# Kernel optimization log

Measured on AMD Instinct MI355X. Metric: run time of the kernel, lower is better.

The kernel has to match this reference:

```python
import jax, jax.numpy as jnp
import numpy as np

N, E, G = 50000, 1600000, 64          # nodes, edges, graphs
NODE_IN, EDGE_IN, HID, L, H = 32, 16, 64, 3, 4
C = HID // H                           # per-head channels (PyG out_channels)


def setup_inputs() -> dict:
    key = jax.random.key(0)
    ks = jax.random.split(key, 12)
    x = jax.random.normal(ks[0], (N, NODE_IN), jnp.float32)
    edge_index = jax.random.randint(ks[1], (2, E), 0, N, jnp.int32)
    edge_attr = jax.random.normal(ks[2], (E, EDGE_IN), jnp.float32)
    batch = jnp.sort(jax.random.randint(ks[3], (N,), 0, G, jnp.int32))
    s = lambda k, shape, fan: jax.random.normal(k, shape, jnp.float32) / np.sqrt(fan)
    Wn = s(ks[4], (NODE_IN, HID), NODE_IN); bn = jnp.zeros((HID,), jnp.float32)
    Wq = s(ks[5], (L, HID, HID), HID);      bq = jnp.zeros((L, HID), jnp.float32)
    Wk = s(ks[6], (L, HID, HID), HID);      bk = jnp.zeros((L, HID), jnp.float32)
    Wv = s(ks[7], (L, HID, HID), HID);      bv = jnp.zeros((L, HID), jnp.float32)
    We = s(ks[8], (L, EDGE_IN, HID), EDGE_IN)          # lin_edge, bias=False in PyG
    Ws = s(ks[9], (L, HID, HID), HID);      bs = jnp.zeros((L, HID), jnp.float32)  # lin_skip
    W1 = s(ks[10], (HID, HID // 2), HID);   b1 = jnp.zeros((HID // 2,), jnp.float32)
    W2 = s(ks[11], (HID // 2, 1), HID // 2); b2 = jnp.zeros((1,), jnp.float32)
    return dict(x=x, edge_index=edge_index, edge_attr=edge_attr, batch=batch,
                Wn=Wn, bn=bn, Wq=Wq, bq=bq, Wk=Wk, bk=bk, Wv=Wv, bv=bv,
                We=We, Ws=Ws, bs=bs, W1=W1, b1=b1, W2=W2, b2=b2)


def _transformer_conv(x, src, dst, edge_attr, Wq, bq, Wk, bk, Wv, bv, We, Ws, bs):
    # PyG TransformerConv (concat=True, beta=False, root_weight=True), eval mode.
    q = (x @ Wq + bq)[dst].reshape(E, H, C)              # query at target nodes
    e = (edge_attr @ We).reshape(E, H, C)                # edge embedding
    k = (x @ Wk + bk)[src].reshape(E, H, C) + e          # key at source + edge
    alpha = (q * k).sum(-1) / jnp.sqrt(jnp.float32(C))   # [E, H]
    amax = jax.ops.segment_max(alpha, dst, num_segments=N)
    ex = jnp.exp(alpha - amax[dst])
    denom = jax.ops.segment_sum(ex, dst, num_segments=N)
    attn = ex / (denom[dst] + 1e-16)                     # segment softmax over in-edges
    v = (x @ Wv + bv)[src].reshape(E, H, C) + e
    agg = jax.ops.segment_sum((v * attn[..., None]).reshape(E, HID), dst, num_segments=N)
    return agg + x @ Ws + bs                             # skip connection (lin_skip)


def reference(x, edge_index, edge_attr, batch, Wn, bn, Wq, bq, Wk, bk, Wv, bv,
              We, Ws, bs, W1, b1, W2, b2):
    src, dst = edge_index[0], edge_index[1]
    h = jax.nn.relu(x @ Wn + bn)
    for l in range(L):  # dropout is identity in eval mode
        h_new = jax.nn.relu(_transformer_conv(h, src, dst, edge_attr,
                                              Wq[l], bq[l], Wk[l], bk[l],
                                              Wv[l], bv[l], We[l], Ws[l], bs[l]))
        h = h + h_new
    # global_mean_pool
    cnt = jax.ops.segment_sum(jnp.ones((N,), h.dtype), batch, num_segments=G)
    pooled = jax.ops.segment_sum(h, batch, num_segments=G) / jnp.maximum(cnt, 1.0)[:, None]
    out = jax.nn.relu(pooled @ W1 + b1) @ W2 + b2
    return out.squeeze(-1)
```

## Files before the change

kernel.cpp:

```cpp
#include <hip/hip_runtime.h>
#include <hip/hip_fp16.h>
#include <stdint.h>

#define Nn 50000
#define Ee 1600000
#define Gg 64
#define TB 2048
#define NTB ((Ee + TB - 1) / TB)
#define NBK ((Nn + 255) / 256)

__global__ void k_hist(const int* __restrict__ ei, int* __restrict__ deg) {
    int e = blockIdx.x * blockDim.x + threadIdx.x;
    if (e < Ee) atomicAdd(&deg[ei[Ee + e]], 1);
}

__global__ void k_scan1(const int* __restrict__ deg, int* __restrict__ row_ptr,
                        int* __restrict__ bsum) {
    __shared__ int buf[256];
    int i = blockIdx.x * 256 + threadIdx.x;
    int v = (i < Nn) ? deg[i] : 0;
    buf[threadIdx.x] = v;
    __syncthreads();
    for (int off = 1; off < 256; off <<= 1) {
        int t = (threadIdx.x >= off) ? buf[threadIdx.x - off] : 0;
        __syncthreads();
        buf[threadIdx.x] += t;
        __syncthreads();
    }
    if (i < Nn) row_ptr[i + 1] = buf[threadIdx.x];
    if (threadIdx.x == 255) bsum[blockIdx.x] = buf[255];
}

__global__ void k_scan2(int* __restrict__ bsum, int nb) {
    __shared__ int buf[256];
    int v = (threadIdx.x < nb) ? bsum[threadIdx.x] : 0;
    buf[threadIdx.x] = v;
    __syncthreads();
    for (int off = 1; off < 256; off <<= 1) {
        int t = (threadIdx.x >= off) ? buf[threadIdx.x - off] : 0;
        __syncthreads();
        buf[threadIdx.x] += t;
        __syncthreads();
    }
    if (threadIdx.x < nb) bsum[threadIdx.x] = buf[threadIdx.x];
}

__global__ void k_scan3(int* __restrict__ row_ptr, const int* __restrict__ bsum) {
    int i = blockIdx.x * 256 + threadIdx.x;
    if (i > Nn) return;
    if (i == 0) { row_ptr[0] = 0; return; }
    int b = (i - 1) >> 8;
    if (b > 0) row_ptr[i] += bsum[b - 1];
}

__global__ void k_scatter(const int* __restrict__ ei, int* __restrict__ cursor,
                          int* __restrict__ src_perm, int* __restrict__ eperm) {
    int e = blockIdx.x * blockDim.x + threadIdx.x;
    if (e >= Ee) return;
    int dst = ei[Ee + e];
    int pos = atomicAdd(&cursor[dst], 1);
    src_perm[pos] = ei[e];
    eperm[pos] = e;
}

__global__ void k_easort(const float* __restrict__ ea, const int* __restrict__ eperm,
                         __half* __restrict__ ea_h) {
    long t = (long)blockIdx.x * blockDim.x + threadIdx.x;
    if (t >= (long)Ee * 4) return;
    long idx = t >> 2;
    int e = eperm[idx];
    float4 v = ((const float4*)ea)[(long)e * 4 + (t & 3)];
    __half2 lo = __floats2half2_rn(v.x, v.y);
    __half2 hi = __floats2half2_rn(v.z, v.w);
    ((__half2*)ea_h)[t * 2]     = lo;
    ((__half2*)ea_h)[t * 2 + 1] = hi;
}


__global__ __launch_bounds__(256) void k_cnt(const int* __restrict__ ei,
                                             int* __restrict__ table) {
    __shared__ int hist[NBK];
    for (int i = threadIdx.x; i < NBK; i += 256) hist[i] = 0;
    __syncthreads();
    int e0 = blockIdx.x * TB;
    for (int i = threadIdx.x; i < TB; i += 256) {
        int e = e0 + i;
        if (e >= Ee) break;
        atomicAdd(&hist[ei[Ee + e] >> 8], 1);
    }
    __syncthreads();
    for (int i = threadIdx.x; i < NBK; i += 256)
        table[i * NTB + blockIdx.x] = hist[i];
}

__global__ __launch_bounds__(256) void k_colscan(int* __restrict__ table,
                                                 int* __restrict__ bktsz) {
    __shared__ int buf[1024];
    int c = blockIdx.x;
    for (int k = 0; k < 4; ++k) {
        int i = threadIdx.x + k * 256;
        buf[i] = (i < NTB) ? table[c * NTB + i] : 0;
    }
    __syncthreads();
    for (int off = 1; off < 1024; off <<= 1) {
        int v[4];
        for (int k = 0; k < 4; ++k) {
            int i = threadIdx.x + k * 256;
            v[k] = (i >= off) ? buf[i - off] : 0;
        }
        __syncthreads();
        for (int k = 0; k < 4; ++k) buf[threadIdx.x + k * 256] += v[k];
        __syncthreads();
    }
    for (int k = 0; k < 4; ++k) {
        int i = threadIdx.x + k * 256;
        if (i < NTB) table[c * NTB + i] = i ? buf[i - 1] : 0;
    }
    if (threadIdx.x == 0) bktsz[c] = buf[1023];
}

__global__ __launch_bounds__(256) void k_bktscan(const int* __restrict__ bktsz,
                                                 int* __restrict__ bktbase) {
    __shared__ int buf[256];
    int i = threadIdx.x;
    buf[i] = (i < NBK) ? bktsz[i] : 0;
    __syncthreads();
    for (int off = 1; off < 256; off <<= 1) {
        int v = (i >= off) ? buf[i - off] : 0;
        __syncthreads();
        buf[i] += v;
        __syncthreads();
    }
    if (i == 0) bktbase[0] = 0;
    if (i < NBK) bktbase[i + 1] = buf[i];
}

__global__ __launch_bounds__(256) void k_binfill(const int* __restrict__ ei,
                        const int* __restrict__ table, const int* __restrict__ bktbase,
                        unsigned long long* __restrict__ tmp) {
    __shared__ int off_s[NBK];
    __shared__ int cnt_s[NBK];
    for (int i = threadIdx.x; i < NBK; i += 256) {
        off_s[i] = table[i * NTB + blockIdx.x];
        cnt_s[i] = 0;
    }
    __syncthreads();
    int e0 = blockIdx.x * TB;
    for (int i = threadIdx.x; i < TB; i += 256) {
        int e = e0 + i;
        if (e >= Ee) break;
        int src = ei[e];
        int dst = ei[Ee + e];
        int b = dst >> 8;
        int r = atomicAdd(&cnt_s[b], 1);
        long pos = (long)bktbase[b] + off_s[b] + r;
        tmp[pos] = ((unsigned long long)(unsigned)dst << 37)
                 | ((unsigned long long)(unsigned)src << 21)
                 | (unsigned long long)(unsigned)e;
    }
}

__global__ __launch_bounds__(256) void k_bktB(const unsigned long long* __restrict__ tmp,
                        const int* __restrict__ bktbase, int* __restrict__ row_ptr,
                        unsigned long long* __restrict__ tmp2) {
    __shared__ int cnt[256];
    __shared__ int sc[256];
    __shared__ int lro[256];
    int b = blockIdx.x, tid = threadIdx.x;
    cnt[tid] = 0;
    __syncthreads();
    int s = bktbase[b], t_end = bktbase[b + 1];
    for (int i = s + tid; i < t_end; i += 256)
        atomicAdd(&cnt[(int)(tmp[i] >> 37) & 255], 1);
    __syncthreads();
    sc[tid] = cnt[tid];
    __syncthreads();
    for (int off = 1; off < 256; off <<= 1) {
        int v = (tid >= off) ? sc[tid - off] : 0;
        __syncthreads();
        sc[tid] += v;
        __syncthreads();
    }
    lro[tid] = tid ? sc[tid - 1] : 0;
    cnt[tid] = 0;
    int n = b * 256 + tid;
    if (n < Nn) row_ptr[n] = s + lro[tid];
    if (b == NBK - 1 && tid == 0) row_ptr[Nn] = Ee;
    __syncthreads();
    for (int i = s + tid; i < t_end; i += 256) {
        unsigned long long p = tmp[i];
        int dn = (int)(p >> 37) & 255;
        int r = atomicAdd(&cnt[dn], 1);
        int pos = s + lro[dn] + r;
        tmp2[pos] = (((p >> 21) & 0xFFFFull) << 32) | (p & 0x1FFFFFull);
    }
}

__global__ void k_scatB(const unsigned long long* __restrict__ tmp2,
                        int* __restrict__ src_perm,
                        const float* __restrict__ ea, __half* __restrict__ ea_h) {
    int t = blockIdx.x * blockDim.x + threadIdx.x;
    if (t >= Ee) return;
    unsigned long long p = tmp2[t];
    src_perm[t] = (int)(p >> 32);
    int e = (int)(p & 0xFFFFFFFFull);
    const float4* er = (const float4*)(ea + (size_t)e * 16);
    float4 v0 = er[0], v1 = er[1], v2 = er[2], v3 = er[3];
    __half2 h0 = __floats2half2_rn(v0.x, v0.y), h1 = __floats2half2_rn(v0.z, v0.w);
    __half2 h2 = __floats2half2_rn(v1.x, v1.y), h3 = __floats2half2_rn(v1.z, v1.w);
    __half2 h4 = __floats2half2_rn(v2.x, v2.y), h5 = __floats2half2_rn(v2.z, v2.w);
    __half2 h6 = __floats2half2_rn(v3.x, v3.y), h7 = __floats2half2_rn(v3.z, v3.w);
    uint4 a = make_uint4(*(unsigned*)&h0, *(unsigned*)&h1,
                         *(unsigned*)&h2, *(unsigned*)&h3);
    uint4 bb = make_uint4(*(unsigned*)&h4, *(unsigned*)&h5,
                          *(unsigned*)&h6, *(unsigned*)&h7);
    uint4* o = (uint4*)(ea_h + (size_t)t * 16);
    o[0] = a;
    o[1] = bb;
}

__global__ void k_gbound(const int* __restrict__ batch, int* __restrict__ gstart) {
    int n = blockIdx.x * blockDim.x + threadIdx.x;
    if (n >= Nn) return;
    int b = batch[n];
    if (n == 0) { for (int g = 0; g <= b; ++g) gstart[g] = 0; }
    else { int bp = batch[n - 1]; for (int g = bp + 1; g <= b; ++g) gstart[g] = n; }
    if (n == Nn - 1) { for (int g = b + 1; g <= Gg; ++g) gstart[g] = Nn; }
}

__global__ __launch_bounds__(256) void k_encode(const float* __restrict__ x,
                         const float* __restrict__ Wn,
                         const float* __restrict__ bn, float* __restrict__ h) {
    __shared__ float sx[64 * 32];
    int base = blockIdx.x * 64;
    for (int i = threadIdx.x; i < 512; i += 256) {
        int off = i * 4, row = off >> 5;
        float4 v = (base + row < Nn) ? ((const float4*)(x))[(base * 32 + off) >> 2]
                                     : make_float4(0.f, 0.f, 0.f, 0.f);
        ((float4*)sx)[i] = v;
    }
    __syncthreads();
    int lane = threadIdx.x & 63, wv = threadIdx.x >> 6;
    float acc[16];
    float b = bn[lane];
#pragma unroll
    for (int nn = 0; nn < 16; ++nn) acc[nn] = b;
#pragma unroll 1
    for (int k0 = 0; k0 < 32; k0 += 4) {
        float w0 = Wn[(k0 + 0) * 64 + lane];
        float w1 = Wn[(k0 + 1) * 64 + lane];
        float w2 = Wn[(k0 + 2) * 64 + lane];
        float w3 = Wn[(k0 + 3) * 64 + lane];
#pragma unroll
        for (int nn = 0; nn < 16; ++nn) {
            int row = wv * 16 + nn;
            float4 hv = *(const float4*)&sx[row * 32 + k0];
            acc[nn] = fmaf(hv.x, w0, fmaf(hv.y, w1, fmaf(hv.z, w2, fmaf(hv.w, w3, acc[nn]))));
        }
    }
#pragma unroll
    for (int nn = 0; nn < 16; ++nn) {
        int n = base + wv * 16 + nn;
        if (n < Nn) h[(size_t)n * 64 + lane] = fmaxf(acc[nn], 0.f);
    }
}

__global__ void k_wqm3(const float* __restrict__ Wq_all, const float* __restrict__ bq_all,
                       const float* __restrict__ We_all, float* __restrict__ Wqm3,
                       float* __restrict__ bqm3) {
    int l = blockIdx.x;
    const float* Wq = Wq_all + l * 4096;
    const float* bq = bq_all + l * 64;
    const float* We = We_all + l * 1024;
    float* Wqm = Wqm3 + l * 4096;
    float* bqm = bqm3 + l * 64;
    for (int o = threadIdx.x; o < 64 * 64; o += 256) {
        int j = o >> 6, lp = o & 63, hh = lp >> 4, ii = lp & 15;
        float acc = 0.f;
#pragma unroll
        for (int c = 0; c < 16; ++c)
            acc += Wq[j * 64 + hh * 16 + c] * We[ii * 64 + hh * 16 + c];
        Wqm[o] = acc;
    }
    if (threadIdx.x < 64) {
        int hh = threadIdx.x >> 4, ii = threadIdx.x & 15;
        float acc = 0.f;
#pragma unroll
        for (int c = 0; c < 16; ++c)
            acc += bq[hh * 16 + c] * We[ii * 64 + hh * 16 + c];
        bqm[threadIdx.x] = acc;
    }
}

__global__ __launch_bounds__(256) void k_qkvt(const float* __restrict__ h,
                       const float* __restrict__ Wq, const float* __restrict__ bq,
                       const float* __restrict__ Wk, const float* __restrict__ bk,
                       const float* __restrict__ Wv, const float* __restrict__ bv,
                       const float* __restrict__ Wqm, const float* __restrict__ bqm,
                       const float* __restrict__ Ws, const float* __restrict__ bs,
                       float* __restrict__ qn, __half* __restrict__ kv,
                       float* __restrict__ tq, float* __restrict__ sn) {
    __shared__ float sh[64 * 64];
    int base = blockIdx.x * 64;
    for (int i = threadIdx.x; i < 1024; i += 256) {
        int off = i * 4, row = off >> 6;
        float4 v = (base + row < Nn) ? ((const float4*)(h))[((size_t)base * 64 + off) >> 2]
                                     : make_float4(0.f, 0.f, 0.f, 0.f);
        ((float4*)sh)[i] = v;
    }
    __syncthreads();
    int lane = threadIdx.x & 63, wv = threadIdx.x >> 6;
    float aq[16], ak[16], av[16], at[16], as_[16];
    float _bq = bq[lane], _bk = bk[lane], _bv = bv[lane], _bt = bqm[lane], _bs = bs[lane];
#pragma unroll
    for (int nn = 0; nn < 16; ++nn) {
        aq[nn] = _bq; ak[nn] = _bk; av[nn] = _bv; at[nn] = _bt; as_[nn] = _bs;
    }
#pragma unroll 1
    for (int k0 = 0; k0 < 64; k0 += 4) {
        float wq[4], wk[4], wvv[4], wt[4], ws[4];
#pragma unroll
        for (int j = 0; j < 4; ++j) {
            wq[j] = Wq[(k0 + j) * 64 + lane];
            wk[j] = Wk[(k0 + j) * 64 + lane];
            wvv[j] = Wv[(k0 + j) * 64 + lane];
            wt[j] = Wqm[(k0 + j) * 64 + lane];
            ws[j] = Ws[(k0 + j) * 64 + lane];
        }
#pragma unroll
        for (int nn = 0; nn < 16; ++nn) {
            int row = wv * 16 + nn;
            float4 hv = *(const float4*)&sh[row * 64 + k0];
            aq[nn] = fmaf(hv.x, wq[0], fmaf(hv.y, wq[1], fmaf(hv.z, wq[2], fmaf(hv.w, wq[3], aq[nn]))));
            ak[nn] = fmaf(hv.x, wk[0], fmaf(hv.y, wk[1], fmaf(hv.z, wk[2], fmaf(hv.w, wk[3], ak[nn]))));
            av[nn] = fmaf(hv.x, wvv[0], fmaf(hv.y, wvv[1], fmaf(hv.z, wvv[2], fmaf(hv.w, wvv[3], av[nn]))));
            at[nn] = fmaf(hv.x, wt[0], fmaf(hv.y, wt[1], fmaf(hv.z, wt[2], fmaf(hv.w, wt[3], at[nn]))));
            as_[nn] = fmaf(hv.x, ws[0], fmaf(hv.y, ws[1], fmaf(hv.z, ws[2], fmaf(hv.w, ws[3], as_[nn]))));
        }
    }
#pragma unroll
    for (int nn = 0; nn < 16; ++nn) {
        int n = base + wv * 16 + nn;
        if (n < Nn) {
            size_t o = (size_t)n * 64 + lane;
            qn[o] = aq[nn]; tq[o] = at[nn]; sn[o] = as_[nn];
            kv[(size_t)n * 128 + lane]      = __float2half_rn(ak[nn]);
            kv[(size_t)n * 128 + 64 + lane] = __float2half_rn(av[nn]);
        }
    }
}

template <bool SORTED>
__global__ __launch_bounds__(256) void k_layer(float* __restrict__ h,
                      const float* __restrict__ qn, const __half* __restrict__ kv,
                      const float* __restrict__ tq, const float* __restrict__ sn,
                      const int* __restrict__ row_ptr, const int* __restrict__ src_perm,
                      const int* __restrict__ eperm, const __half* __restrict__ eah,
                      const float* __restrict__ eaf, const float* __restrict__ We) {
    __shared__ float sWe[1024];
    __shared__ float tile[4][64];
    for (int t = threadIdx.x; t < 1024; t += 256) sWe[t] = We[t];
    __syncthreads();
    int lane = threadIdx.x & 63, wv = threadIdx.x >> 6;
    int hh = lane >> 4, cc = lane & 15;
    int n = blockIdx.x * 4 + wv;
    if (n >= Nn) return;
    int beg = row_ptr[n], end = row_ptr[n + 1];
    const float SC = 0.25f * 1.4426950408889634f;
    float q = qn[(size_t)n * 64 + lane] * SC;
    float t = tq[(size_t)n * 64 + lane] * SC;
    float m = -INFINITY, accd = 0.f, accv = 0.f, acce = 0.f;
    int idx = beg;
    for (; idx + 4 <= end; idx += 4) {
        long b0 = (long)src_perm[idx] * 128,     b1 = (long)src_perm[idx + 1] * 128;
        long b2 = (long)src_perm[idx + 2] * 128, b3 = (long)src_perm[idx + 3] * 128;
        float k0 = __half2float(kv[b0 + lane]),      k1 = __half2float(kv[b1 + lane]);
        float k2 = __half2float(kv[b2 + lane]),      k3 = __half2float(kv[b3 + lane]);
        float v0 = __half2float(kv[b0 + 64 + lane]), v1 = __half2float(kv[b1 + 64 + lane]);
        float v2 = __half2float(kv[b2 + 64 + lane]), v3 = __half2float(kv[b3 + 64 + lane]);
        float x0, x1, x2, x3;
        if (SORTED) {
            long o0 = (long)idx * 16;
            x0 = __half2float(eah[o0 + cc]);      x1 = __half2float(eah[o0 + 16 + cc]);
            x2 = __half2float(eah[o0 + 32 + cc]); x3 = __half2float(eah[o0 + 48 + cc]);
        } else {
            x0 = eaf[(long)eperm[idx] * 16 + cc];     x1 = eaf[(long)eperm[idx + 1] * 16 + cc];
            x2 = eaf[(long)eperm[idx + 2] * 16 + cc]; x3 = eaf[(long)eperm[idx + 3] * 16 + cc];
        }
        float a0 = fmaf(q, k0, x0 * t), a1 = fmaf(q, k1, x1 * t);
        float a2 = fmaf(q, k2, x2 * t), a3 = fmaf(q, k3, x3 * t);
        a0 += __shfl_xor(a0, 1, 16); a1 += __shfl_xor(a1, 1, 16);
        a2 += __shfl_xor(a2, 1, 16); a3 += __shfl_xor(a3, 1, 16);
        a0 += __shfl_xor(a0, 2, 16); a1 += __shfl_xor(a1, 2, 16);
        a2 += __shfl_xor(a2, 2, 16); a3 += __shfl_xor(a3, 2, 16);
        a0 += __shfl_xor(a0, 4, 16); a1 += __shfl_xor(a1, 4, 16);
        a2 += __shfl_xor(a2, 4, 16); a3 += __shfl_xor(a3, 4, 16);
        a0 += __shfl_xor(a0, 8, 16); a1 += __shfl_xor(a1, 8, 16);
        a2 += __shfl_xor(a2, 8, 16); a3 += __shfl_xor(a3, 8, 16);
        float mx = fmaxf(fmaxf(a0, a1), fmaxf(a2, a3));
        float nm = fmaxf(m, mx);
        float w = __builtin_exp2f(m - nm);
        float p0 = __builtin_exp2f(a0 - nm), p1 = __builtin_exp2f(a1 - nm);
        float p2 = __builtin_exp2f(a2 - nm), p3 = __builtin_exp2f(a3 - nm);
        accd = fmaf(accd, w, (p0 + p1) + (p2 + p3));
        accv = fmaf(accv, w, fmaf(p0, v0, fmaf(p1, v1, fmaf(p2, v2, p3 * v3))));
        acce = fmaf(acce, w, fmaf(p0, x0, fmaf(p1, x1, fmaf(p2, x2, p3 * x3))));
        m = nm;
    }
    for (; idx < end; ++idx) {
        long b0 = (long)src_perm[idx] * 128;
        float k0 = __half2float(kv[b0 + lane]);
        float v0 = __half2float(kv[b0 + 64 + lane]);
        float x0 = SORTED ? __half2float(eah[(long)idx * 16 + cc])
                          : eaf[(long)eperm[idx] * 16 + cc];
        float a0 = fmaf(q, k0, x0 * t);
        a0 += __shfl_xor(a0, 1, 16);
        a0 += __shfl_xor(a0, 2, 16);
        a0 += __shfl_xor(a0, 4, 16);
        a0 += __shfl_xor(a0, 8, 16);
        float nm = fmaxf(m, a0);
        float w = __builtin_exp2f(m - nm);
        float p0 = __builtin_exp2f(a0 - nm);
        accd = fmaf(accd, w, p0);
        accv = fmaf(accv, w, p0 * v0);
        acce = fmaf(acce, w, p0 * x0);
        m = nm;
    }
    float inv = 1.f / (accd + 1e-16f);
    tile[wv][lane] = acce * inv;
    float re = 0.f;
#pragma unroll
    for (int i = 0; i < 16; ++i)
        re = fmaf(tile[wv][hh * 16 + i], sWe[i * 64 + lane], re);
    size_t o = (size_t)n * 64 + lane;
    float hv = h[o];
    h[o] = hv + fmaxf(fmaf(accv, inv, re + sn[o]), 0.f);
}

__global__ void k_pool(const float* __restrict__ h, const int* __restrict__ gstart,
                       const float* __restrict__ W1, const float* __restrict__ b1,
                       const float* __restrict__ W2, const float* __restrict__ b2,
                       float* __restrict__ out) {
    int g = blockIdx.x;
    int lane = threadIdx.x & 63, wv = threadIdx.x >> 6;
    int beg = gstart[g], end = gstart[g + 1];
    __shared__ float red[4][64];
    __shared__ float sp[64];
    __shared__ float sh[32];
    float acc = 0.f;
    for (int n = beg + wv; n < end; n += 4) acc += h[(size_t)n * 64 + lane];
    red[wv][lane] = acc;
    __syncthreads();
    if (threadIdx.x < 64) {
        float c = fmaxf((float)(end - beg), 1.f);
        sp[lane] = (red[0][lane] + red[1][lane] + red[2][lane] + red[3][lane]) / c;
    }
    __syncthreads();
    if (threadIdx.x < 32) {
        int t = threadIdx.x;
        float a = b1[t];
#pragma unroll
        for (int i = 0; i < 64; ++i) a = fmaf(sp[i], W1[i * 32 + t], a);
        sh[t] = fmaxf(a, 0.f) * W2[t];
    }
    __syncthreads();
    if (threadIdx.x == 0) {
        float s = b2[0];
#pragma unroll
        for (int i = 0; i < 32; ++i) s += sh[i];
        out[g] = s;
    }
}

extern "C" void kernel_launch(void* const* d_in, const int* in_sizes, int n_in,
                              void* d_out, int out_size, void* d_ws, size_t ws_size,
                              hipStream_t stream) {
    const float* x   = (const float*)d_in[0];
    const int*   ei  = (const int*)d_in[1];
    const float* ea  = (const float*)d_in[2];
    const int*   bat = (const int*)d_in[3];
    const float* Wn  = (const float*)d_in[4];
    const float* bn  = (const float*)d_in[5];
    const float* Wq  = (const float*)d_in[6];
    const float* bq  = (const float*)d_in[7];
    const float* Wk  = (const float*)d_in[8];
    const float* bk  = (const float*)d_in[9];
    const float* Wv  = (const float*)d_in[10];
    const float* bv  = (const float*)d_in[11];
    const float* We  = (const float*)d_in[12];
    const float* Wsk = (const float*)d_in[13];
    const float* bs  = (const float*)d_in[14];
    const float* W1  = (const float*)d_in[15];
    const float* b1  = (const float*)d_in[16];
    const float* W2  = (const float*)d_in[17];
    const float* b2  = (const float*)d_in[18];
    float* out = (float*)d_out;

    const size_t NH = (size_t)Nn * 64;
    float* h    = (float*)d_ws;
    float* qn   = h + NH;
    float* tq   = h + 2 * NH;
    float* sn   = h + 3 * NH;
    __half* kv  = (__half*)(h + 4 * NH);
    float* Wqm3 = h + 5 * NH;
    float* bqm3 = Wqm3 + 3 * 4096;
    int* deg       = (int*)(bqm3 + 3 * 64);
    int* row_ptr   = deg + Nn;
    int* cursor    = row_ptr + Nn + 1;
    int* src_perm  = cursor + Nn;
    int* eperm     = src_perm + Ee;
    int* bsum      = eperm + Ee;
    int* gstart    = bsum + 256;
    char* pe = (char*)(gstart + Gg + 1);
    __half* ea_h = (__half*)(((uintptr_t)pe + 63) & ~(uintptr_t)63);
    char* pt = (char*)(ea_h + (size_t)Ee * 16);
    unsigned long long* tmp =
        (unsigned long long*)(((uintptr_t)pt + 15) & ~(uintptr_t)15);
    size_t need_eah = ((char*)(ea_h + (size_t)Ee * 16)) - (char*)d_ws;
    size_t need_tmp = ((char*)(tmp + Ee)) - (char*)d_ws;
    unsigned long long* tmp2 = (unsigned long long*)qn;
    int* table   = (int*)tq;
    int* bktsz   = (int*)sn;
    int* bktbase = bktsz + 256;
    int mode = (ws_size >= need_tmp) ? 2 : (ws_size >= need_eah) ? 1 : 0;

    if (mode == 2) {
        k_cnt<<<NTB, 256, 0, stream>>>(ei, table);
        k_colscan<<<NBK, 256, 0, stream>>>(table, bktsz);
        k_bktscan<<<1, 256, 0, stream>>>(bktsz, bktbase);
        k_binfill<<<NTB, 256, 0, stream>>>(ei, table, bktbase, tmp);
        k_bktB<<<NBK, 256, 0, stream>>>(tmp, bktbase, row_ptr, tmp2);
        k_scatB<<<(Ee + 255) / 256, 256, 0, stream>>>(tmp2, src_perm, ea, ea_h);
    } else {
        const int NB = 196;
        hipMemsetAsync(deg, 0, Nn * sizeof(int), stream);
        k_hist<<<(Ee + 255) / 256, 256, 0, stream>>>(ei, deg);
        k_scan1<<<NB, 256, 0, stream>>>(deg, row_ptr, bsum);
        k_scan2<<<1, 256, 0, stream>>>(bsum, NB);
        k_scan3<<<(Nn + 256) / 256, 256, 0, stream>>>(row_ptr, bsum);
        hipMemcpyAsync(cursor, row_ptr, Nn * sizeof(int), hipMemcpyDeviceToDevice, stream);
        k_scatter<<<(Ee + 255) / 256, 256, 0, stream>>>(ei, cursor, src_perm, eperm);
        if (mode == 1)
            k_easort<<<((long)Ee * 4 + 255) / 256, 256, 0, stream>>>(ea, eperm, ea_h);
    }
    k_gbound<<<(Nn + 255) / 256, 256, 0, stream>>>(bat, gstart);
    k_wqm3<<<3, 256, 0, stream>>>(Wq, bq, We, Wqm3, bqm3);

    int nodeBlocks = (Nn + 63) / 64;
    k_encode<<<nodeBlocks, 256, 0, stream>>>(x, Wn, bn, h);
    bool sorted = mode >= 1;
    for (int l = 0; l < 3; ++l) {
        k_qkvt<<<nodeBlocks, 256, 0, stream>>>(h, Wq + l * 4096, bq + l * 64,
                                               Wk + l * 4096, bk + l * 64,
                                               Wv + l * 4096, bv + l * 64,
                                               Wqm3 + l * 4096, bqm3 + l * 64,
                                               Wsk + l * 4096, bs + l * 64,
                                               qn, kv, tq, sn);
        if (sorted)
            k_layer<true><<<(Nn + 3) / 4, 256, 0, stream>>>(h, qn, kv, tq, sn,
                    row_ptr, src_perm, eperm, ea_h, ea, We + l * 1024);
        else
            k_layer<false><<<(Nn + 3) / 4, 256, 0, stream>>>(h, qn, kv, tq, sn,
                    row_ptr, src_perm, eperm, ea_h, ea, We + l * 1024);
    }
    k_pool<<<Gg, 256, 0, stream>>>(h, gstart, W1, b1, W2, b2, out);
}
```

Measured before the change: 770.3 us.

## Process two edges per wavefront with half2 loads in sorted-edge layer kernel

New measurement: 725.2 us. 5.9% less time.

```diff
diff --git a/kernel.cpp b/kernel.cpp
--- a/kernel.cpp
+++ b/kernel.cpp
@@ -350,6 +350,78 @@
     }
 }
 
+__global__ __launch_bounds__(256) void k_layer2(float* __restrict__ h,
+                      const float* __restrict__ qn, const __half* __restrict__ kv,
+                      const float* __restrict__ tq, const float* __restrict__ sn,
+                      const int* __restrict__ row_ptr, const int* __restrict__ src_perm,
+                      const __half* __restrict__ eah, const float* __restrict__ We) {
+    __shared__ float sWe[1024];
+    __shared__ float tE[4][64];
+    __shared__ float tV[4][64];
+    for (int t = threadIdx.x; t < 1024; t += 256) sWe[t] = We[t];
+    __syncthreads();
+    int lane = threadIdx.x & 63, wv = threadIdx.x >> 6;
+    int slot = lane >> 5, sl = lane & 31;
+    int n = blockIdx.x * 4 + wv;
+    if (n >= Nn) return;
+    int beg = row_ptr[n], end = row_ptr[n + 1];
+    const float SC = 0.25f * 1.4426950408889634f;
+    float2 q2 = *(const float2*)&qn[(size_t)n * 64 + 2 * sl];
+    float2 t2 = *(const float2*)&tq[(size_t)n * 64 + 2 * sl];
+    q2.x *= SC; q2.y *= SC; t2.x *= SC; t2.y *= SC;
+    const __half2* kv2 = (const __half2*)kv;
+    const __half2* ea2 = (const __half2*)eah;
+    float m = -INFINITY, accd = 0.f;
+    float2 accv = make_float2(0.f, 0.f), acce = make_float2(0.f, 0.f);
+    for (int idx = beg; idx < end; idx += 4) {
+        int e0 = idx + slot, e1 = idx + 2 + slot;
+        bool ok0 = e0 < end, ok1 = e1 < end;
+        int i0 = ok0 ? e0 : beg, i1 = ok1 ? e1 : beg;
+        int s0 = src_perm[i0], s1 = src_perm[i1];
+        float2 k0 = __half22float2(kv2[s0 * 64 + sl]);
+        float2 v0 = __half22float2(kv2[s0 * 64 + 32 + sl]);
+        float2 k1 = __half22float2(kv2[s1 * 64 + sl]);
+        float2 v1 = __half22float2(kv2[s1 * 64 + 32 + sl]);
+        float2 x0 = __half22float2(ea2[(size_t)i0 * 8 + (sl & 7)]);
+        float2 x1 = __half22float2(ea2[(size_t)i1 * 8 + (sl & 7)]);
+        float a0 = fmaf(q2.x, k0.x, fmaf(q2.y, k0.y, fmaf(t2.x, x0.x, t2.y * x0.y)));
+        float a1 = fmaf(q2.x, k1.x, fmaf(q2.y, k1.y, fmaf(t2.x, x1.x, t2.y * x1.y)));
+        a0 += __shfl_xor(a0, 1, 8); a1 += __shfl_xor(a1, 1, 8);
+        a0 += __shfl_xor(a0, 2, 8); a1 += __shfl_xor(a1, 2, 8);
+        a0 += __shfl_xor(a0, 4, 8); a1 += __shfl_xor(a1, 4, 8);
+        if (!ok0) a0 = -INFINITY;
+        if (!ok1) a1 = -INFINITY;
+        float b0 = __shfl_xor(a0, 32), b1 = __shfl_xor(a1, 32);
+        float nm = fmaxf(m, fmaxf(fmaxf(a0, b0), fmaxf(a1, b1)));
+        float w = __builtin_exp2f(m - nm);
+        float p0 = __builtin_exp2f(a0 - nm), p1 = __builtin_exp2f(a1 - nm);
+        accd = fmaf(accd, w, p0 + p1);
+        accv.x = fmaf(accv.x, w, fmaf(p0, v0.x, p1 * v1.x));
+        accv.y = fmaf(accv.y, w, fmaf(p0, v0.y, p1 * v1.y));
+        acce.x = fmaf(acce.x, w, fmaf(p0, x0.x, p1 * x1.x));
+        acce.y = fmaf(acce.y, w, fmaf(p0, x0.y, p1 * x1.y));
+        m = nm;
+    }
+    accd   += __shfl_xor(accd, 32);
+    accv.x += __shfl_xor(accv.x, 32);
+    accv.y += __shfl_xor(accv.y, 32);
+    acce.x += __shfl_xor(acce.x, 32);
+    acce.y += __shfl_xor(acce.y, 32);
+    float inv = 1.f / (accd + 1e-16f);
+    if (slot == 0) {
+        ((float2*)tE[wv])[sl] = make_float2(acce.x * inv, acce.y * inv);
+        ((float2*)tV[wv])[sl] = make_float2(accv.x * inv, accv.y * inv);
+    }
+    int hh = lane >> 4;
+    float re = 0.f;
+#pragma unroll
+    for (int i = 0; i < 16; ++i)
+        re = fmaf(tE[wv][hh * 16 + i], sWe[i * 64 + lane], re);
+    size_t o = (size_t)n * 64 + lane;
+    float hv = h[o];
+    h[o] = hv + fmaxf(tV[wv][lane] + re + sn[o], 0.f);
+}
+
 template <bool SORTED>
 __global__ __launch_bounds__(256) void k_layer(float* __restrict__ h,
                       const float* __restrict__ qn, const __half* __restrict__ kv,
@@ -371,42 +443,6 @@
     float t = tq[(size_t)n * 64 + lane] * SC;
     float m = -INFINITY, accd = 0.f, accv = 0.f, acce = 0.f;
     int idx = beg;
-    for (; idx + 4 <= end; idx += 4) {
-        long b0 = (long)src_perm[idx] * 128,     b1 = (long)src_perm[idx + 1] * 128;
-        long b2 = (long)src_perm[idx + 2] * 128, b3 = (long)src_perm[idx + 3] * 128;
-        float k0 = __half2float(kv[b0 + lane]),      k1 = __half2float(kv[b1 + lane]);
-        float k2 = __half2float(kv[b2 + lane]),      k3 = __half2float(kv[b3 + lane]);
-        float v0 = __half2float(kv[b0 + 64 + lane]), v1 = __half2float(kv[b1 + 64 + lane]);
-        float v2 = __half2float(kv[b2 + 64 + lane]), v3 = __half2float(kv[b3 + 64 + lane]);
-        float x0, x1, x2, x3;
-        if (SORTED) {
-            long o0 = (long)idx * 16;
-            x0 = __half2float(eah[o0 + cc]);      x1 = __half2float(eah[o0 + 16 + cc]);
-            x2 = __half2float(eah[o0 + 32 + cc]); x3 = __half2float(eah[o0 + 48 + cc]);
-        } else {
-            x0 = eaf[(long)eperm[idx] * 16 + cc];     x1 = eaf[(long)eperm[idx + 1] * 16 + cc];
-            x2 = eaf[(long)eperm[idx + 2] * 16 + cc]; x3 = eaf[(long)eperm[idx + 3] * 16 + cc];
-        }
-        float a0 = fmaf(q, k0, x0 * t), a1 = fmaf(q, k1, x1 * t);
-        float a2 = fmaf(q, k2, x2 * t), a3 = fmaf(q, k3, x3 * t);
-        a0 += __shfl_xor(a0, 1, 16); a1 += __shfl_xor(a1, 1, 16);
-        a2 += __shfl_xor(a2, 1, 16); a3 += __shfl_xor(a3, 1, 16);
-        a0 += __shfl_xor(a0, 2, 16); a1 += __shfl_xor(a1, 2, 16);
-        a2 += __shfl_xor(a2, 2, 16); a3 += __shfl_xor(a3, 2, 16);
-        a0 += __shfl_xor(a0, 4, 16); a1 += __shfl_xor(a1, 4, 16);
-        a2 += __shfl_xor(a2, 4, 16); a3 += __shfl_xor(a3, 4, 16);
-        a0 += __shfl_xor(a0, 8, 16); a1 += __shfl_xor(a1, 8, 16);
-        a2 += __shfl_xor(a2, 8, 16); a3 += __shfl_xor(a3, 8, 16);
-        float mx = fmaxf(fmaxf(a0, a1), fmaxf(a2, a3));
-        float nm = fmaxf(m, mx);
-        float w = __builtin_exp2f(m - nm);
-        float p0 = __builtin_exp2f(a0 - nm), p1 = __builtin_exp2f(a1 - nm);
-        float p2 = __builtin_exp2f(a2 - nm), p3 = __builtin_exp2f(a3 - nm);
-        accd = fmaf(accd, w, (p0 + p1) + (p2 + p3));
-        accv = fmaf(accv, w, fmaf(p0, v0, fmaf(p1, v1, fmaf(p2, v2, p3 * v3))));
-        acce = fmaf(acce, w, fmaf(p0, x0, fmaf(p1, x1, fmaf(p2, x2, p3 * x3))));
-        m = nm;
-    }
     for (; idx < end; ++idx) {
         long b0 = (long)src_perm[idx] * 128;
         float k0 = __half2float(kv[b0 + lane]);
@@ -548,7 +584,6 @@
 
     int nodeBlocks = (Nn + 63) / 64;
     k_encode<<<nodeBlocks, 256, 0, stream>>>(x, Wn, bn, h);
-    bool sorted = mode >= 1;
     for (int l = 0; l < 3; ++l) {
         k_qkvt<<<nodeBlocks, 256, 0, stream>>>(h, Wq + l * 4096, bq + l * 64,
                                                Wk + l * 4096, bk + l * 64,
@@ -556,9 +591,9 @@
                                                Wqm3 + l * 4096, bqm3 + l * 64,
                                                Wsk + l * 4096, bs + l * 64,
                                                qn, kv, tq, sn);
-        if (sorted)
-            k_layer<true><<<(Nn + 3) / 4, 256, 0, stream>>>(h, qn, kv, tq, sn,
-                    row_ptr, src_perm, eperm, ea_h, ea, We + l * 1024);
+        if (mode >= 1)
+            k_layer2<<<(Nn + 3) / 4, 256, 0, stream>>>(h, qn, kv, tq, sn,
+                    row_ptr, src_perm, ea_h, We + l * 1024);
         else
             k_layer<false><<<(Nn + 3) / 4, 256, 0, stream>>>(h, qn, kv, tq, sn,
                     row_ptr, src_perm, eperm, ea_h, ea, We + l * 1024);
```
